# Kernel tuning notes

Measured on AMD Instinct MI355X. Metric: run time of the kernel, lower is better.

The kernel has to match this reference:

```python
import jax, jax.numpy as jnp
import numpy as np

B, T, IN, H = 16, 1024, 1024, 1024


def setup_inputs() -> dict:
    key = jax.random.key(0)
    ks = jax.random.split(key, 6)
    s_in = 1.0 / np.sqrt(IN)
    s_out = 1.0 / np.sqrt(2 * H)
    return {
        "x": jax.random.normal(ks[0], (B, T, IN), jnp.float32),
        "W_in": jax.random.uniform(ks[1], (H, IN), jnp.float32, -s_in, s_in),
        "b_in": jax.random.uniform(ks[2], (H,), jnp.float32, -s_in, s_in),
        "leak_tau_v": jax.random.normal(ks[3], (H,), jnp.float32),
        "flip_threshold": jnp.full((H,), 0.5, jnp.float32),
        "W_out": jax.random.uniform(ks[4], (H, 2 * H), jnp.float32, -s_out, s_out),
        "b_out": jax.random.uniform(ks[5], (H,), jnp.float32, -s_out, s_out),
    }


def _hsru_scan(I_tbh, alpha, thr):
    """Leaky-integrate / threshold-reset recurrence over time.
    I_tbh: [T,B,H]; alpha, thr: [H]. Returns (v_seq, spike_seq) each [T,B,H].
    v_t = alpha*v_{t-1} + I_t; spike on crossing threshold; v reset on spike.
    """
    def step(v, I_t):
        v = alpha * v + I_t
        spike = (v > thr).astype(v.dtype)  # hard threshold; zero grad (as in torch)
        v = v * (1.0 - spike)              # reset membrane on flip
        return v, (v, spike)

    v0 = jnp.zeros(I_tbh.shape[1:], I_tbh.dtype)
    _, (v_seq, s_seq) = jax.lax.scan(step, v0, I_tbh)
    return v_seq, s_seq


def reference(x, W_in, b_in, leak_tau_v, flip_threshold, W_out, b_out):
    # input currents: [B,T,H]
    I = jnp.einsum('bti,hi->bth', x, W_in) + b_in
    alpha = jnp.exp(-jax.nn.softplus(leak_tau_v))  # [H], in (0,1)
    v_seq, s_seq = _hsru_scan(jnp.swapaxes(I, 0, 1), alpha, flip_threshold)
    combined = jnp.concatenate([v_seq, s_seq], axis=-1)   # [T,B,2H]
    combined = jnp.swapaxes(combined, 0, 1)               # [B,T,2H]
    return jnp.tanh(jnp.einsum('btk,hk->bth', combined, W_out) + b_out)
```

## Files before the change

kernel.cpp:

```cpp
#include <hip/hip_runtime.h>
#include <hip/hip_bf16.h>
#include <cmath>


typedef __attribute__((ext_vector_type(8))) __bf16 bf16x8;
typedef __attribute__((ext_vector_type(4))) __bf16 bf16x4;
typedef __attribute__((ext_vector_type(4))) float  f32x4;

#define LDT 40
#define LDF 36

__global__ __launch_bounds__(256)
void gemm1_f32chain_kernel(const float* __restrict__ X,
                           const float* __restrict__ W,
                           const float* __restrict__ bias,
                           float* __restrict__ I)
{
    __shared__ __align__(16) float sA[128][LDF];
    __shared__ __align__(16) float sB[128][LDF];

    const int tid  = threadIdx.x;
    const int bn   = blockIdx.x;
    const int bm   = blockIdx.y;
    const int row0 = bm * 128;
    const int col0 = bn * 128;
    const int tx   = tid & 15;
    const int ty   = tid >> 4;

    float acc[8][8];
    #pragma unroll
    for (int i = 0; i < 8; ++i)
        #pragma unroll
        for (int j = 0; j < 8; ++j)
            acc[i][j] = 0.0f;

    for (int k0 = 0; k0 < 1024; k0 += 32) {
        #pragma unroll
        for (int i = 0; i < 4; ++i) {
            int q  = tid + i * 256;
            int r  = q >> 3;
            int c4 = (q & 7) * 4;
            *(f32x4*)&sA[r][c4] = *(const f32x4*)&X[(size_t)(row0 + r) * 1024 + k0 + c4];
            *(f32x4*)&sB[r][c4] = *(const f32x4*)&W[(size_t)(col0 + r) * 1024 + k0 + c4];
        }
        __syncthreads();

        #pragma unroll
        for (int kk = 0; kk < 32; kk += 4) {
            f32x4 a4[8], b4[8];
            #pragma unroll
            for (int i = 0; i < 8; ++i) a4[i] = *(const f32x4*)&sA[ty + 16 * i][kk];
            #pragma unroll
            for (int j = 0; j < 8; ++j) b4[j] = *(const f32x4*)&sB[tx + 16 * j][kk];
            #pragma unroll
            for (int q = 0; q < 4; ++q)
                #pragma unroll
                for (int i = 0; i < 8; ++i)
                    #pragma unroll
                    for (int j = 0; j < 8; ++j)
                        acc[i][j] = fmaf(a4[i][q], b4[j][q], acc[i][j]);
        }
        __syncthreads();
    }

    #pragma unroll
    for (int i = 0; i < 8; ++i)
        #pragma unroll
        for (int j = 0; j < 8; ++j) {
            int rg = row0 + ty + 16 * i;
            int cg = col0 + tx + 16 * j;
            I[(size_t)rg * 1024 + cg] = __fadd_rn(acc[i][j], bias[cg]);
        }
}

__global__ void hsru_scan_f32_kernel(const float* __restrict__ I,
                                     const float* __restrict__ leak,
                                     const float* __restrict__ thr,
                                     __bf16* __restrict__ comb)
{
    int g = blockIdx.x * blockDim.x + threadIdx.x;
    int b = g >> 10;
    int h = g & 1023;

    float lt = leak[h];
    float e     = (float)exp(-(double)fabsf(lt));
    float l1    = (float)log1p((double)e);
    float sp    = __fadd_rn(fmaxf(lt, 0.0f), l1);
    float alpha = (float)exp(-(double)sp);
    float th    = thr[h];

    const float* Ip = I    + (size_t)b * (1024 * 1024) + h;
    __bf16*      cp = comb + (size_t)b * (1024 * 2048) + h;

    float v = 0.0f;
    #pragma unroll 4
    for (int t = 0; t < 1024; ++t) {
        float cur = Ip[(size_t)t * 1024];
        v = __fadd_rn(__fmul_rn(alpha, v), cur);
        float spike = (v > th) ? 1.0f : 0.0f;
        v = __fmul_rn(v, __fsub_rn(1.0f, spike));
        cp[(size_t)t * 2048]        = (__bf16)v;
        cp[(size_t)t * 2048 + 1024] = (__bf16)spike;
    }
}

__global__ __launch_bounds__(256)
void gemm2_kernel(const __bf16* __restrict__ A,
                  const float* __restrict__ W,
                  const float* __restrict__ bias,
                  float* __restrict__ O)
{
    __shared__ __align__(16) __bf16 sA[128][LDT];
    __shared__ __align__(16) __bf16 sB[128][LDT];

    const int tid  = threadIdx.x;
    const int bn   = blockIdx.x;
    const int bm   = blockIdx.y;
    const int row0 = bm * 128;
    const int col0 = bn * 128;

    const int lane = tid & 63;
    const int wid  = tid >> 6;
    const int wm   = (wid >> 1) * 64;
    const int wn   = (wid & 1) * 64;

    f32x4 acc[4][4];
    #pragma unroll
    for (int i = 0; i < 4; ++i)
        #pragma unroll
        for (int j = 0; j < 4; ++j)
            acc[i][j] = f32x4{0.f, 0.f, 0.f, 0.f};

    const int frow  = lane & 15;
    const int fkoff = (lane >> 4) * 8;

    for (int k0 = 0; k0 < 2048; k0 += 32) {
        #pragma unroll
        for (int i = 0; i < 2; ++i) {
            int q  = tid + i * 256;
            int r  = q >> 2;
            int c8 = (q & 3) * 8;
            *(bf16x8*)&sA[r][c8] = *(const bf16x8*)&A[(size_t)(row0 + r) * 2048 + k0 + c8];
        }
        #pragma unroll
        for (int i = 0; i < 4; ++i) {
            int q  = tid + i * 256;
            int r  = q >> 3;
            int c4 = (q & 7) * 4;
            const f32x4 vb = *(const f32x4*)&W[(size_t)(col0 + r) * 2048 + k0 + c4];
            bf16x4 bh;
            #pragma unroll
            for (int j = 0; j < 4; ++j) bh[j] = (__bf16)vb[j];
            *(bf16x4*)&sB[r][c4] = bh;
        }
        __syncthreads();

        bf16x8 a_f[4], b_f[4];
        #pragma unroll
        for (int f = 0; f < 4; ++f) {
            a_f[f] = *(const bf16x8*)&sA[wm + f * 16 + frow][fkoff];
            b_f[f] = *(const bf16x8*)&sB[wn + f * 16 + frow][fkoff];
        }
        #pragma unroll
        for (int fm = 0; fm < 4; ++fm)
            #pragma unroll
            for (int fn = 0; fn < 4; ++fn)
                acc[fm][fn] = __builtin_amdgcn_mfma_f32_16x16x32_bf16(a_f[fm], b_f[fn], acc[fm][fn], 0, 0, 0);
        __syncthreads();
    }

    const int crow = (lane >> 4) * 4;
    const int ccol = lane & 15;
    #pragma unroll
    for (int fm = 0; fm < 4; ++fm)
        #pragma unroll
        for (int fn = 0; fn < 4; ++fn)
            #pragma unroll
            for (int j = 0; j < 4; ++j) {
                int rg = row0 + wm + fm * 16 + crow + j;
                int cg = col0 + wn + fn * 16 + ccol;
                O[(size_t)rg * 1024 + cg] = tanhf(acc[fm][fn][j] + bias[cg]);
            }
}

extern "C" void kernel_launch(void* const* d_in, const int* in_sizes, int n_in,
                              void* d_out, int out_size, void* d_ws, size_t ws_size,
                              hipStream_t stream)
{
    const float* x     = (const float*)d_in[0];
    const float* W_in  = (const float*)d_in[1];
    const float* b_in  = (const float*)d_in[2];
    const float* leak  = (const float*)d_in[3];
    const float* thr   = (const float*)d_in[4];
    const float* W_out = (const float*)d_in[5];
    const float* b_out = (const float*)d_in[6];

    const size_t NEED = 64ull * 1024 * 1024;
    if (ws_size < NEED) return;

    float*  out  = (float*)d_out;
    __bf16* comb = (__bf16*)d_ws;

    dim3 grid(8, 128);

    gemm1_f32chain_kernel<<<grid, 256, 0, stream>>>(x, W_in, b_in, out);
    hsru_scan_f32_kernel<<<64, 256, 0, stream>>>(out, leak, thr, comb);
    gemm2_kernel<<<grid, 256, 0, stream>>>(comb, W_out, b_out, out);
}
```

Before: 654.8 us.

## Register-prefetch GEMM1 tiles and pre-convert W_out to bf16 once per call

```diff
diff --git a/kernel.cpp b/kernel.cpp
--- a/kernel.cpp
+++ b/kernel.cpp
@@ -27,6 +27,16 @@
     const int tx   = tid & 15;
     const int ty   = tid >> 4;
 
+    int rr[4], cc[4];
+    #pragma unroll
+    for (int i = 0; i < 4; ++i) {
+        int q = tid + i * 256;
+        rr[i] = q >> 3;
+        cc[i] = (q & 7) * 4;
+    }
+
+    f32x4 av[4], bv[4];
+
     float acc[8][8];
     #pragma unroll
     for (int i = 0; i < 8; ++i)
@@ -34,16 +44,29 @@
         for (int j = 0; j < 8; ++j)
             acc[i][j] = 0.0f;
 
+    #pragma unroll
+    for (int i = 0; i < 4; ++i) {
+        av[i] = *(const f32x4*)&X[(size_t)(row0 + rr[i]) * 1024 + cc[i]];
+        bv[i] = *(const f32x4*)&W[(size_t)(col0 + rr[i]) * 1024 + cc[i]];
+    }
+
     for (int k0 = 0; k0 < 1024; k0 += 32) {
+        __syncthreads();
         #pragma unroll
         for (int i = 0; i < 4; ++i) {
-            int q  = tid + i * 256;
-            int r  = q >> 3;
-            int c4 = (q & 7) * 4;
-            *(f32x4*)&sA[r][c4] = *(const f32x4*)&X[(size_t)(row0 + r) * 1024 + k0 + c4];
-            *(f32x4*)&sB[r][c4] = *(const f32x4*)&W[(size_t)(col0 + r) * 1024 + k0 + c4];
-        }
-        __syncthreads();
+            *(f32x4*)&sA[rr[i]][cc[i]] = av[i];
+            *(f32x4*)&sB[rr[i]][cc[i]] = bv[i];
+        }
+        __syncthreads();
+
+        if (k0 + 32 < 1024) {
+            const int kn = k0 + 32;
+            #pragma unroll
+            for (int i = 0; i < 4; ++i) {
+                av[i] = *(const f32x4*)&X[(size_t)(row0 + rr[i]) * 1024 + kn + cc[i]];
+                bv[i] = *(const f32x4*)&W[(size_t)(col0 + rr[i]) * 1024 + kn + cc[i]];
+            }
+        }
 
         #pragma unroll
         for (int kk = 0; kk < 32; kk += 4) {
@@ -60,7 +83,6 @@
                     for (int j = 0; j < 8; ++j)
                         acc[i][j] = fmaf(a4[i][q], b4[j][q], acc[i][j]);
         }
-        __syncthreads();
     }
 
     #pragma unroll
@@ -105,8 +127,20 @@
 }
 
 __global__ __launch_bounds__(256)
+void wcvt_kernel(const float* __restrict__ W, __bf16* __restrict__ Wb)
+{
+    int idx = (blockIdx.x * 256 + threadIdx.x) * 8;
+    f32x4 v0 = *(const f32x4*)&W[idx];
+    f32x4 v1 = *(const f32x4*)&W[idx + 4];
+    bf16x8 o;
+    #pragma unroll
+    for (int j = 0; j < 4; ++j) { o[j] = (__bf16)v0[j]; o[4 + j] = (__bf16)v1[j]; }
+    *(bf16x8*)&Wb[idx] = o;
+}
+
+__global__ __launch_bounds__(256)
 void gemm2_kernel(const __bf16* __restrict__ A,
-                  const float* __restrict__ W,
+                  const __bf16* __restrict__ Wb,
                   const float* __restrict__ bias,
                   float* __restrict__ O)
 {
@@ -140,18 +174,8 @@
             int q  = tid + i * 256;
             int r  = q >> 2;
             int c8 = (q & 3) * 8;
-            *(bf16x8*)&sA[r][c8] = *(const bf16x8*)&A[(size_t)(row0 + r) * 2048 + k0 + c8];
-        }
-        #pragma unroll
-        for (int i = 0; i < 4; ++i) {
-            int q  = tid + i * 256;
-            int r  = q >> 3;
-            int c4 = (q & 7) * 4;
-            const f32x4 vb = *(const f32x4*)&W[(size_t)(col0 + r) * 2048 + k0 + c4];
-            bf16x4 bh;
-            #pragma unroll
-            for (int j = 0; j < 4; ++j) bh[j] = (__bf16)vb[j];
-            *(bf16x4*)&sB[r][c4] = bh;
+            *(bf16x8*)&sA[r][c8] = *(const bf16x8*)&A [(size_t)(row0 + r) * 2048 + k0 + c8];
+            *(bf16x8*)&sB[r][c8] = *(const bf16x8*)&Wb[(size_t)(col0 + r) * 2048 + k0 + c8];
         }
         __syncthreads();
 
@@ -195,15 +219,17 @@
     const float* W_out = (const float*)d_in[5];
     const float* b_out = (const float*)d_in[6];
 
-    const size_t NEED = 64ull * 1024 * 1024;
+    const size_t NEED = (64ull << 20) + (4ull << 20);
     if (ws_size < NEED) return;
 
     float*  out  = (float*)d_out;
     __bf16* comb = (__bf16*)d_ws;
+    __bf16* Wb   = (__bf16*)((char*)d_ws + (64ull << 20));
 
     dim3 grid(8, 128);
 
+    wcvt_kernel<<<1024, 256, 0, stream>>>(W_out, Wb);
     gemm1_f32chain_kernel<<<grid, 256, 0, stream>>>(x, W_in, b_in, out);
     hsru_scan_f32_kernel<<<64, 256, 0, stream>>>(out, leak, thr, comb);
-    gemm2_kernel<<<grid, 256, 0, stream>>>(comb, W_out, b_out, out);
-}
+    gemm2_kernel<<<grid, 256, 0, stream>>>(comb, Wb, b_out, out);
+}
```

After: 663.0 us. About the same (+1.3%).
